# Kernel tuning notes

Measured on AMD Instinct MI355X. Metric: run time of the kernel, lower is better.

Reference implementation:

```python
import jax, jax.numpy as jnp
import numpy as np

V, E, H = 50257, 512, 1024
B, S = 64, 512


def setup_inputs() -> dict:
    key = jax.random.key(0)
    ks = jax.random.split(key, 12)
    return {
        "inp": jax.random.randint(ks[0], (B,), 0, V),
        "hidden": jax.random.normal(ks[1], (1, B, H), dtype=jnp.float32),
        "encoder_outputs": jax.random.normal(ks[2], (B, S, H), dtype=jnp.float32),
        "emb": jax.random.normal(ks[3], (V, E), dtype=jnp.float32) * 0.02,
        "W": jax.random.uniform(ks[4], (H, H), dtype=jnp.float32) - 0.5,
        "U": jax.random.uniform(ks[5], (H, H), dtype=jnp.float32) - 0.5,
        "v": jax.random.uniform(ks[6], (H, 1), dtype=jnp.float32) - 0.5,
        "W_ih": jax.random.normal(ks[7], (H, E), dtype=jnp.float32) * 0.02,
        "W_hh": jax.random.normal(ks[8], (H, H), dtype=jnp.float32) * 0.02,
        "b_ih": jnp.zeros((H,), dtype=jnp.float32),
        "b_hh": jnp.zeros((H,), dtype=jnp.float32),
        "out_W": jax.random.normal(ks[9], (V, H), dtype=jnp.float32) * 0.02,
        "out_b": jnp.zeros((V,), dtype=jnp.float32),
    }


def reference(inp, hidden, encoder_outputs, emb, W, U, v, W_ih, W_hh, b_ih, b_hh, out_W, out_b):
    # Embedding lookup: (B, E)
    x = emb[inp]
    # Bahdanau additive attention. last decoder state: hidden[0] -> (B, H)
    Wh = jnp.einsum('ij,bsj->bis', W, encoder_outputs)        # (B, H, S)
    Uh = jnp.einsum('ij,bj->bi', U, hidden[0])[:, :, None]    # (B, H, 1)
    e = jnp.einsum('h,bhs->bs', v[:, 0], jnp.tanh(Wh + Uh))   # (B, S)
    alpha = jax.nn.softmax(e, axis=-1)                        # exp_e / sum(exp_e)
    context = jnp.einsum('bs,bsh->bh', alpha, encoder_outputs)  # (B, H)
    # Single-step tanh RNN with the attention context as initial hidden state
    h = jnp.tanh(x @ W_ih.T + b_ih + context @ W_hh.T + b_hh)  # (B, H)
    logits = h @ out_W.T + out_b                                # (B, V)
    # Match torch shapes: rnn_output (B,1,H) -> logits (B,1,V); h_n (1,B,H)
    return logits[:, None, :], h[None, :, :]
```

## Files before the change

### kernel.cpp

```cpp
#include <hip/hip_runtime.h>
#include <hip/hip_bf16.h>
#include <stdint.h>

#define DEVINL __device__ __forceinline__

typedef __bf16 bf16x8 __attribute__((ext_vector_type(8)));
typedef float  f32x4  __attribute__((ext_vector_type(4)));
typedef unsigned int uint2v __attribute__((ext_vector_type(2)));
typedef unsigned int uint4v __attribute__((ext_vector_type(4)));
typedef unsigned short ushort_t;

#define VSZ   50257
#define EDIM  512
#define HDIM  1024
#define BATCH 64
#define SEQ   512


DEVINL f32x4 MF(bf16x8 a, bf16x8 b, f32x4 c) {
  return __builtin_amdgcn_mfma_f32_16x16x32_bf16(a, b, c, 0, 0, 0);
}

DEVINL bf16x8 ldfrag(const short* buf, int row, int k) {
  uint4v t = *(const uint4v*)&buf[row * 64 + (k ^ ((row & 7) << 3))];
  return __builtin_bit_cast(bf16x8, t);
}

DEVINL void split4(f32x4 w, uint2v& hv, uint2v& lv) {
  unsigned u0 = __float_as_uint(w.x), u1 = __float_as_uint(w.y);
  unsigned u2 = __float_as_uint(w.z), u3 = __float_as_uint(w.w);
  unsigned h0 = u0 & 0xFFFF0000u, h1 = u1 & 0xFFFF0000u;
  unsigned h2 = u2 & 0xFFFF0000u, h3 = u3 & 0xFFFF0000u;
  hv.x = (h0 >> 16) | h1;
  hv.y = (h2 >> 16) | h3;
  float l0 = w.x - __uint_as_float(h0);
  float l1 = w.y - __uint_as_float(h1);
  float l2 = w.z - __uint_as_float(h2);
  float l3 = w.w - __uint_as_float(h3);
  lv.x = (__float_as_uint(l0) >> 16) | (__float_as_uint(l1) & 0xFFFF0000u);
  lv.y = (__float_as_uint(l2) >> 16) | (__float_as_uint(l3) & 0xFFFF0000u);
}

DEVINL uint2v packhi4_rn(f32x4 w) {
  unsigned u0 = __float_as_uint(w.x), u1 = __float_as_uint(w.y);
  unsigned u2 = __float_as_uint(w.z), u3 = __float_as_uint(w.w);
  unsigned r0 = u0 + 0x7FFFu + ((u0 >> 16) & 1u);
  unsigned r1 = u1 + 0x7FFFu + ((u1 >> 16) & 1u);
  unsigned r2 = u2 + 0x7FFFu + ((u2 >> 16) & 1u);
  unsigned r3 = u3 + 0x7FFFu + ((u3 >> 16) & 1u);
  uint2v o;
  o.x = (r0 >> 16) | (r1 & 0xFFFF0000u);
  o.y = (r2 >> 16) | (r3 & 0xFFFF0000u);
  return o;
}

DEVINL float fast_tanh(float s) {
  float e2 = __expf(2.0f * s);
  return 1.0f - 2.0f * __builtin_amdgcn_rcpf(e2 + 1.0f);
}

__global__ __launch_bounds__(256) void prep_w_kernel(const float* __restrict__ W,
                                                     ushort_t* __restrict__ Whi,
                                                     ushort_t* __restrict__ Wlo) {
  int idx4 = blockIdx.x * 256 + threadIdx.x;
  f32x4 w = *(const f32x4*)&W[(size_t)idx4 * 4];
  uint2v hv, lv;
  split4(w, hv, lv);
  ((uint2v*)Whi)[idx4] = hv;
  ((uint2v*)Wlo)[idx4] = lv;
}

__global__ __launch_bounds__(256) void uh_kernel(const float* __restrict__ U,
                                                 const float* __restrict__ hidden,
                                                 float* __restrict__ Uh) {
  int wid = threadIdx.x >> 6, lane = threadIdx.x & 63;
  int i = blockIdx.x * 4 + wid;
  const float* Urow = U + (size_t)i * HDIM;
  float acc[64];
#pragma unroll
  for (int b = 0; b < 64; ++b) acc[b] = 0.0f;
  for (int t = 0; t < HDIM / 64; ++t) {
    float w = Urow[t * 64 + lane];
#pragma unroll
    for (int b = 0; b < 64; ++b)
      acc[b] += w * hidden[(size_t)b * HDIM + t * 64 + lane];
  }
#pragma unroll
  for (int mask = 1; mask <= 32; mask <<= 1)
#pragma unroll
    for (int b = 0; b < 64; ++b) acc[b] += __shfl_xor(acc[b], mask, 64);
  if (lane == 0) {
#pragma unroll
    for (int b = 0; b < 64; ++b) Uh[(size_t)b * HDIM + i] = acc[b];
  }
}

__global__ __launch_bounds__(256) void e_kernel(const float* __restrict__ enc,
                                                const ushort_t* __restrict__ Whi,
                                                const ushort_t* __restrict__ Wlo,
                                                const float* __restrict__ Uh,
                                                const float* __restrict__ v,
                                                float* __restrict__ e_parts) {
  __shared__ short Ahi[128 * 64], Alo[128 * 64], Bhi[128 * 64], Blo[128 * 64];
  __shared__ float ewave[2][2][64];

  const int t = threadIdx.x;
  const int i0 = blockIdx.x * 128;
  const int bs0 = blockIdx.y * 128;
  const int wid = t >> 6, lane = t & 63, r = lane & 15, g = lane >> 4;
  const int wr = wid >> 1, wc = wid & 1;

  f32x4 z4 = {0.f, 0.f, 0.f, 0.f};
  f32x4 acc[4][4];
#pragma unroll
  for (int m = 0; m < 4; ++m)
#pragma unroll
    for (int n = 0; n < 4; ++n) acc[m][n] = z4;

  for (int kt = 0; kt < 16; ++kt) {
    __syncthreads();
#pragma unroll
    for (int rep = 0; rep < 8; ++rep) {
      int p = rep * 256 + t;
      int row = p >> 4, c = p & 15;
      f32x4 w = *(const f32x4*)&enc[(size_t)(bs0 + row) * HDIM + kt * 64 + c * 4];
      uint2v hv, lv;
      split4(w, hv, lv);
      int idx = row * 64 + ((c * 4) ^ ((row & 7) << 3));
      *(uint2v*)&Ahi[idx] = hv;
      *(uint2v*)&Alo[idx] = lv;
    }
#pragma unroll
    for (int rep = 0; rep < 4; ++rep) {
      int p = rep * 256 + t;
      int row = p >> 3, c = p & 7;
      int idx = row * 64 + ((c * 8) ^ ((row & 7) << 3));
      *(uint4v*)&Bhi[idx] = *(const uint4v*)&Whi[(size_t)(i0 + row) * HDIM + kt * 64 + c * 8];
      *(uint4v*)&Blo[idx] = *(const uint4v*)&Wlo[(size_t)(i0 + row) * HDIM + kt * 64 + c * 8];
    }
    __syncthreads();
#pragma unroll
    for (int ks = 0; ks < 2; ++ks) {
      int k = ks * 32 + g * 8;
      bf16x8 ah[4], al[4], bh[4], bl[4];
#pragma unroll
      for (int m = 0; m < 4; ++m) {
        int arow = wr * 64 + m * 16 + r;
        ah[m] = ldfrag(Ahi, arow, k);
        al[m] = ldfrag(Alo, arow, k);
        int brow = wc * 64 + m * 16 + r;
        bh[m] = ldfrag(Bhi, brow, k);
        bl[m] = ldfrag(Blo, brow, k);
      }
#pragma unroll
      for (int m = 0; m < 4; ++m)
#pragma unroll
        for (int n = 0; n < 4; ++n) {
          acc[m][n] = MF(ah[m], bh[n], acc[m][n]);
          acc[m][n] = MF(ah[m], bl[n], acc[m][n]);
          acc[m][n] = MF(al[m], bh[n], acc[m][n]);
        }
    }
  }

  const int b = bs0 >> 9;
  float uhv[4], vv[4];
#pragma unroll
  for (int n = 0; n < 4; ++n) {
    int col = i0 + wc * 64 + n * 16 + r;
    uhv[n] = Uh[(size_t)b * HDIM + col];
    vv[n] = v[col];
  }
  float esum[16];
#pragma unroll
  for (int q = 0; q < 16; ++q) esum[q] = 0.0f;
#pragma unroll
  for (int m = 0; m < 4; ++m)
#pragma unroll
    for (int n = 0; n < 4; ++n)
#pragma unroll
      for (int j = 0; j < 4; ++j) {
        float s = acc[m][n][j] + uhv[n];
        esum[m * 4 + j] += fast_tanh(s) * vv[n];
      }
#pragma unroll
  for (int mask = 1; mask <= 8; mask <<= 1)
#pragma unroll
    for (int q = 0; q < 16; ++q) esum[q] += __shfl_xor(esum[q], mask, 64);
  if (r == 0) {
#pragma unroll
    for (int m = 0; m < 4; ++m)
#pragma unroll
      for (int j = 0; j < 4; ++j)
        ewave[wr][wc][m * 16 + g * 4 + j] = esum[m * 4 + j];
  }
  __syncthreads();
  if (t < 128) {
    int w2 = t >> 6, rr = t & 63;
    e_parts[(size_t)blockIdx.x * 32768 + bs0 + w2 * 64 + rr] =
        ewave[w2][0][rr] + ewave[w2][1][rr];
  }
}

__global__ __launch_bounds__(256) void softmax_kernel(const float* __restrict__ e_parts,
                                                      float* __restrict__ alpha) {
  __shared__ float red[256];
  int b = blockIdx.x, t = threadIdx.x;
  float ev0 = 0.f, ev1 = 0.f;
#pragma unroll
  for (int nc = 0; nc < 8; ++nc) {
    ev0 += e_parts[(size_t)nc * 32768 + b * SEQ + t];
    ev1 += e_parts[(size_t)nc * 32768 + b * SEQ + t + 256];
  }
  red[t] = fmaxf(ev0, ev1);
  __syncthreads();
  for (int off = 128; off > 0; off >>= 1) {
    if (t < off) red[t] = fmaxf(red[t], red[t + off]);
    __syncthreads();
  }
  float mx = red[0];
  __syncthreads();
  float x0 = __expf(ev0 - mx), x1 = __expf(ev1 - mx);
  red[t] = x0 + x1;
  __syncthreads();
  for (int off = 128; off > 0; off >>= 1) {
    if (t < off) red[t] += red[t + off];
    __syncthreads();
  }
  float inv = 1.0f / red[0];
  alpha[b * SEQ + t] = x0 * inv;
  alpha[b * SEQ + t + 256] = x1 * inv;
}

__global__ __launch_bounds__(256) void ctx_kernel(const float* __restrict__ alpha,
                                                  const float* __restrict__ enc,
                                                  float* __restrict__ ctx_parts) {
  int b = blockIdx.x, q = blockIdx.y, t = threadIdx.x;
  f32x4 acc = {0.f, 0.f, 0.f, 0.f};
  for (int s = q * 128; s < q * 128 + 128; ++s) {
    float a = alpha[b * SEQ + s];
    f32x4 ev = *(const f32x4*)&enc[((size_t)b * SEQ + s) * HDIM + t * 4];
    acc.x += a * ev.x; acc.y += a * ev.y; acc.z += a * ev.z; acc.w += a * ev.w;
  }
  *(f32x4*)&ctx_parts[((size_t)q * BATCH + b) * HDIM + t * 4] = acc;
}

__global__ __launch_bounds__(256) void ctx_reduce_kernel(const float* __restrict__ ctx_parts,
                                                         float* __restrict__ ctx) {
  int idx = blockIdx.x * 256 + threadIdx.x;
  const f32x4* p = (const f32x4*)ctx_parts;
  f32x4 s0 = p[idx];
  f32x4 s1 = p[idx + 16384];
  f32x4 s2 = p[idx + 32768];
  f32x4 s3 = p[idx + 49152];
  f32x4 r;
  r.x = s0.x + s1.x + s2.x + s3.x;
  r.y = s0.y + s1.y + s2.y + s3.y;
  r.z = s0.z + s1.z + s2.z + s3.z;
  r.w = s0.w + s1.w + s2.w + s3.w;
  ((f32x4*)ctx)[idx] = r;
}

__global__ __launch_bounds__(256) void rnn_kernel(const int* __restrict__ inp,
                                                  const float* __restrict__ emb,
                                                  const float* __restrict__ Wih,
                                                  const float* __restrict__ Whh,
                                                  const float* __restrict__ bih,
                                                  const float* __restrict__ bhh,
                                                  const float* __restrict__ ctx,
                                                  float* __restrict__ h_out,
                                                  ushort_t* __restrict__ h_bf16) {
  int wid = threadIdx.x >> 6, lane = threadIdx.x & 63;
  int i = blockIdx.x * 4 + wid;
  float acc[64];
#pragma unroll
  for (int b = 0; b < 64; ++b) acc[b] = 0.0f;
  const float* w1 = Wih + (size_t)i * EDIM;
  for (int t = 0; t < EDIM / 64; ++t) {
    float w = w1[t * 64 + lane];
#pragma unroll
    for (int b = 0; b < 64; ++b)
      acc[b] += w * emb[(size_t)inp[b] * EDIM + t * 64 + lane];
  }
  const float* w2 = Whh + (size_t)i * HDIM;
  for (int t = 0; t < HDIM / 64; ++t) {
    float w = w2[t * 64 + lane];
#pragma unroll
    for (int b = 0; b < 64; ++b)
      acc[b] += w * ctx[(size_t)b * HDIM + t * 64 + lane];
  }
#pragma unroll
  for (int mask = 1; mask <= 32; mask <<= 1)
#pragma unroll
    for (int b = 0; b < 64; ++b) acc[b] += __shfl_xor(acc[b], mask, 64);
  if (lane == 0) {
    float bias = bih[i] + bhh[i];
#pragma unroll
    for (int b = 0; b < 64; ++b) {
      float hv = fast_tanh(acc[b] + bias);
      h_out[(size_t)b * HDIM + i] = hv;
      unsigned u = __float_as_uint(hv);
      h_bf16[(size_t)b * HDIM + i] = (ushort_t)((u + 0x7FFFu + ((u >> 16) & 1u)) >> 16);
    }
  }
}

__global__ __launch_bounds__(256) void logits_kernel(const ushort_t* __restrict__ hbf,
                                                     const float* __restrict__ outW,
                                                     const float* __restrict__ outb,
                                                     float* __restrict__ out) {
  __shared__ short As[64 * 64];
  __shared__ short Bs[128 * 64];
  const int t = threadIdx.x;
  const int n0 = blockIdx.x * 128;
  const int wid = t >> 6, lane = t & 63, r = lane & 15, g = lane >> 4;

  f32x4 z4 = {0.f, 0.f, 0.f, 0.f};
  f32x4 acc[4][2];
#pragma unroll
  for (int m = 0; m < 4; ++m) {
    acc[m][0] = z4;
    acc[m][1] = z4;
  }

  for (int kt = 0; kt < 16; ++kt) {
    __syncthreads();
#pragma unroll
    for (int rep = 0; rep < 2; ++rep) {
      int p = rep * 256 + t;
      int row = p >> 3, c = p & 7;
      *(uint4v*)&As[row * 64 + ((c * 8) ^ ((row & 7) << 3))] =
          *(const uint4v*)&hbf[(size_t)row * HDIM + kt * 64 + c * 8];
    }
#pragma unroll
    for (int rep = 0; rep < 8; ++rep) {
      int p = rep * 256 + t;
      int row = p >> 4, c = p & 15;
      int gr = n0 + row;
      f32x4 wv = z4;
      if (gr < VSZ) wv = *(const f32x4*)&outW[(size_t)gr * HDIM + kt * 64 + c * 4];
      *(uint2v*)&Bs[row * 64 + ((c * 4) ^ ((row & 7) << 3))] = packhi4_rn(wv);
    }
    __syncthreads();
#pragma unroll
    for (int ks = 0; ks < 2; ++ks) {
      int k = ks * 32 + g * 8;
      bf16x8 a[4], bb[2];
#pragma unroll
      for (int m = 0; m < 4; ++m) a[m] = ldfrag(As, m * 16 + r, k);
#pragma unroll
      for (int n = 0; n < 2; ++n) bb[n] = ldfrag(Bs, wid * 32 + n * 16 + r, k);
#pragma unroll
      for (int m = 0; m < 4; ++m)
#pragma unroll
        for (int n = 0; n < 2; ++n) acc[m][n] = MF(a[m], bb[n], acc[m][n]);
    }
  }
#pragma unroll
  for (int n = 0; n < 2; ++n) {
    int col = n0 + wid * 32 + n * 16 + r;
    if (col < VSZ) {
      float ob = outb[col];
#pragma unroll
      for (int m = 0; m < 4; ++m)
#pragma unroll
        for (int j = 0; j < 4; ++j) {
          int row = m * 16 + g * 4 + j;
          out[(size_t)row * VSZ + col] = acc[m][n][j] + ob;
        }
    }
  }
}

extern "C" void kernel_launch(void* const* d_in, const int* in_sizes, int n_in,
                              void* d_out, int out_size, void* d_ws, size_t ws_size,
                              hipStream_t stream) {
  const int* inp = (const int*)d_in[0];
  const float* hidden = (const float*)d_in[1];
  const float* enc = (const float*)d_in[2];
  const float* emb = (const float*)d_in[3];
  const float* W = (const float*)d_in[4];
  const float* U = (const float*)d_in[5];
  const float* v = (const float*)d_in[6];
  const float* Wih = (const float*)d_in[7];
  const float* Whh = (const float*)d_in[8];
  const float* bih = (const float*)d_in[9];
  const float* bhh = (const float*)d_in[10];
  const float* outW = (const float*)d_in[11];
  const float* outb = (const float*)d_in[12];
  float* out = (float*)d_out;

  char* ws = (char*)d_ws;
  ushort_t* Whi = (ushort_t*)(ws + 0);
  ushort_t* Wlo = (ushort_t*)(ws + 2097152);
  float* Uh = (float*)(ws + 4194304);
  float* e_parts = (float*)(ws + 4456448);
  float* alpha = (float*)(ws + 5505024);
  float* ctx_parts = (float*)(ws + 5636096);
  float* ctx = (float*)(ws + 6684672);
  ushort_t* hbf = (ushort_t*)(ws + 6946816);

  prep_w_kernel<<<1024, 256, 0, stream>>>(W, Whi, Wlo);
  uh_kernel<<<256, 256, 0, stream>>>(U, hidden, Uh);
  e_kernel<<<dim3(8, 256), 256, 0, stream>>>(enc, Whi, Wlo, Uh, v, e_parts);
  softmax_kernel<<<64, 256, 0, stream>>>(e_parts, alpha);
  ctx_kernel<<<dim3(64, 4), 256, 0, stream>>>(alpha, enc, ctx_parts);
  ctx_reduce_kernel<<<64, 256, 0, stream>>>(ctx_parts, ctx);
  rnn_kernel<<<256, 256, 0, stream>>>(inp, emb, Wih, Whh, bih, bhh, ctx,
                                      out + (size_t)BATCH * VSZ, hbf);
  logits_kernel<<<(VSZ + 127) / 128, 256, 0, stream>>>(hbf, outW, outb, out);
}
```

Measured before the change: 1.022 ms.

## Shrink e_kernel K-tile with padded LDS, widen ctx grid, halve logits tile

Three separate changes. The attention-score GEMM moves from 64-wide K tiles with XOR swizzle to 32-wide K tiles in padded rows of stride 40, which cuts LDS use so more blocks can be resident, at the cost of twice as many sync rounds. The context reduction gets 4x more blocks by also splitting along the hidden dimension, with scalar loads and four independent accumulators. The logits GEMM halves its N tile to 64 columns, doubling the block count for more parallelism but reloading the hidden-state tile more often.

Measured after the change: 832.7 us. 1.23x faster.

```diff
diff --git a/kernel.cpp b/kernel.cpp
--- a/kernel.cpp
+++ b/kernel.cpp
@@ -19,6 +19,11 @@
 
 DEVINL f32x4 MF(bf16x8 a, bf16x8 b, f32x4 c) {
   return __builtin_amdgcn_mfma_f32_16x16x32_bf16(a, b, c, 0, 0, 0);
+}
+
+DEVINL bf16x8 ldfrag40(const short* buf, int row, int k) {
+  uint4v t = *(const uint4v*)&buf[row * 40 + k];
+  return __builtin_bit_cast(bf16x8, t);
 }
 
 DEVINL bf16x8 ldfrag(const short* buf, int row, int k) {
@@ -101,7 +106,7 @@
                                                 const float* __restrict__ Uh,
                                                 const float* __restrict__ v,
                                                 float* __restrict__ e_parts) {
-  __shared__ short Ahi[128 * 64], Alo[128 * 64], Bhi[128 * 64], Blo[128 * 64];
+  __shared__ short Ahi[128 * 40], Alo[128 * 40], Bhi[128 * 40], Blo[128 * 40];
   __shared__ float ewave[2][2][64];
 
   const int t = threadIdx.x;
@@ -117,40 +122,39 @@
 #pragma unroll
     for (int n = 0; n < 4; ++n) acc[m][n] = z4;
 
-  for (int kt = 0; kt < 16; ++kt) {
-    __syncthreads();
-#pragma unroll
-    for (int rep = 0; rep < 8; ++rep) {
-      int p = rep * 256 + t;
-      int row = p >> 4, c = p & 15;
-      f32x4 w = *(const f32x4*)&enc[(size_t)(bs0 + row) * HDIM + kt * 64 + c * 4];
-      uint2v hv, lv;
-      split4(w, hv, lv);
-      int idx = row * 64 + ((c * 4) ^ ((row & 7) << 3));
-      *(uint2v*)&Ahi[idx] = hv;
-      *(uint2v*)&Alo[idx] = lv;
-    }
+  for (int kt = 0; kt < 32; ++kt) {
+    __syncthreads();
 #pragma unroll
     for (int rep = 0; rep < 4; ++rep) {
       int p = rep * 256 + t;
       int row = p >> 3, c = p & 7;
-      int idx = row * 64 + ((c * 8) ^ ((row & 7) << 3));
-      *(uint4v*)&Bhi[idx] = *(const uint4v*)&Whi[(size_t)(i0 + row) * HDIM + kt * 64 + c * 8];
-      *(uint4v*)&Blo[idx] = *(const uint4v*)&Wlo[(size_t)(i0 + row) * HDIM + kt * 64 + c * 8];
-    }
-    __syncthreads();
-#pragma unroll
-    for (int ks = 0; ks < 2; ++ks) {
-      int k = ks * 32 + g * 8;
+      f32x4 w = *(const f32x4*)&enc[(size_t)(bs0 + row) * HDIM + kt * 32 + c * 4];
+      uint2v hv, lv;
+      split4(w, hv, lv);
+      int idx = row * 40 + c * 4;
+      *(uint2v*)&Ahi[idx] = hv;
+      *(uint2v*)&Alo[idx] = lv;
+    }
+#pragma unroll
+    for (int rep = 0; rep < 2; ++rep) {
+      int p = rep * 256 + t;
+      int row = p >> 2, c = p & 3;
+      int idx = row * 40 + c * 8;
+      *(uint4v*)&Bhi[idx] = *(const uint4v*)&Whi[(size_t)(i0 + row) * HDIM + kt * 32 + c * 8];
+      *(uint4v*)&Blo[idx] = *(const uint4v*)&Wlo[(size_t)(i0 + row) * HDIM + kt * 32 + c * 8];
+    }
+    __syncthreads();
+    {
+      int k = g * 8;
       bf16x8 ah[4], al[4], bh[4], bl[4];
 #pragma unroll
       for (int m = 0; m < 4; ++m) {
         int arow = wr * 64 + m * 16 + r;
-        ah[m] = ldfrag(Ahi, arow, k);
-        al[m] = ldfrag(Alo, arow, k);
+        ah[m] = ldfrag40(Ahi, arow, k);
+        al[m] = ldfrag40(Alo, arow, k);
         int brow = wc * 64 + m * 16 + r;
-        bh[m] = ldfrag(Bhi, brow, k);
-        bl[m] = ldfrag(Blo, brow, k);
+        bh[m] = ldfrag40(Bhi, brow, k);
+        bl[m] = ldfrag40(Blo, brow, k);
       }
 #pragma unroll
       for (int m = 0; m < 4; ++m)
@@ -235,14 +239,21 @@
 __global__ __launch_bounds__(256) void ctx_kernel(const float* __restrict__ alpha,
                                                   const float* __restrict__ enc,
                                                   float* __restrict__ ctx_parts) {
-  int b = blockIdx.x, q = blockIdx.y, t = threadIdx.x;
-  f32x4 acc = {0.f, 0.f, 0.f, 0.f};
-  for (int s = q * 128; s < q * 128 + 128; ++s) {
-    float a = alpha[b * SEQ + s];
-    f32x4 ev = *(const f32x4*)&enc[((size_t)b * SEQ + s) * HDIM + t * 4];
-    acc.x += a * ev.x; acc.y += a * ev.y; acc.z += a * ev.z; acc.w += a * ev.w;
-  }
-  *(f32x4*)&ctx_parts[((size_t)q * BATCH + b) * HDIM + t * 4] = acc;
+  int b = blockIdx.x, qs = blockIdx.y, qh = blockIdx.z, t = threadIdx.x;
+  int h = qh * 256 + t;
+  float a0 = 0.f, a1 = 0.f, a2 = 0.f, a3 = 0.f;
+  int s0 = qs * 128;
+  for (int s = s0; s < s0 + 128; s += 4) {
+    float w0 = alpha[b * SEQ + s + 0];
+    float w1 = alpha[b * SEQ + s + 1];
+    float w2 = alpha[b * SEQ + s + 2];
+    float w3 = alpha[b * SEQ + s + 3];
+    a0 += w0 * enc[((size_t)b * SEQ + s + 0) * HDIM + h];
+    a1 += w1 * enc[((size_t)b * SEQ + s + 1) * HDIM + h];
+    a2 += w2 * enc[((size_t)b * SEQ + s + 2) * HDIM + h];
+    a3 += w3 * enc[((size_t)b * SEQ + s + 3) * HDIM + h];
+  }
+  ctx_parts[((size_t)qs * BATCH + b) * HDIM + h] = (a0 + a1) + (a2 + a3);
 }
 
 __global__ __launch_bounds__(256) void ctx_reduce_kernel(const float* __restrict__ ctx_parts,
@@ -310,18 +321,15 @@
                                                      const float* __restrict__ outb,
                                                      float* __restrict__ out) {
   __shared__ short As[64 * 64];
-  __shared__ short Bs[128 * 64];
+  __shared__ short Bs[64 * 64];
   const int t = threadIdx.x;
-  const int n0 = blockIdx.x * 128;
+  const int n0 = blockIdx.x * 64;
   const int wid = t >> 6, lane = t & 63, r = lane & 15, g = lane >> 4;
 
   f32x4 z4 = {0.f, 0.f, 0.f, 0.f};
-  f32x4 acc[4][2];
-#pragma unroll
-  for (int m = 0; m < 4; ++m) {
-    acc[m][0] = z4;
-    acc[m][1] = z4;
-  }
+  f32x4 acc[4];
+#pragma unroll
+  for (int m = 0; m < 4; ++m) acc[m] = z4;
 
   for (int kt = 0; kt < 16; ++kt) {
     __syncthreads();
@@ -333,7 +341,7 @@
           *(const uint4v*)&hbf[(size_t)row * HDIM + kt * 64 + c * 8];
     }
 #pragma unroll
-    for (int rep = 0; rep < 8; ++rep) {
+    for (int rep = 0; rep < 4; ++rep) {
       int p = rep * 256 + t;
       int row = p >> 4, c = p & 15;
       int gr = n0 + row;
@@ -345,20 +353,16 @@
 #pragma unroll
     for (int ks = 0; ks < 2; ++ks) {
       int k = ks * 32 + g * 8;
-      bf16x8 a[4], bb[2];
+      bf16x8 a[4], bb;
 #pragma unroll
       for (int m = 0; m < 4; ++m) a[m] = ldfrag(As, m * 16 + r, k);
-#pragma unroll
-      for (int n = 0; n < 2; ++n) bb[n] = ldfrag(Bs, wid * 32 + n * 16 + r, k);
-#pragma unroll
-      for (int m = 0; m < 4; ++m)
-#pragma unroll
-        for (int n = 0; n < 2; ++n) acc[m][n] = MF(a[m], bb[n], acc[m][n]);
-    }
-  }
-#pragma unroll
-  for (int n = 0; n < 2; ++n) {
-    int col = n0 + wid * 32 + n * 16 + r;
+      bb = ldfrag(Bs, wid * 16 + r, k);
+#pragma unroll
+      for (int m = 0; m < 4; ++m) acc[m] = MF(a[m], bb, acc[m]);
+    }
+  }
+  {
+    int col = n0 + wid * 16 + r;
     if (col < VSZ) {
       float ob = outb[col];
 #pragma unroll
@@ -366,7 +370,7 @@
 #pragma unroll
         for (int j = 0; j < 4; ++j) {
           int row = m * 16 + g * 4 + j;
-          out[(size_t)row * VSZ + col] = acc[m][n][j] + ob;
+          out[(size_t)row * VSZ + col] = acc[m][j] + ob;
         }
     }
   }
@@ -404,9 +408,9 @@
   uh_kernel<<<256, 256, 0, stream>>>(U, hidden, Uh);
   e_kernel<<<dim3(8, 256), 256, 0, stream>>>(enc, Whi, Wlo, Uh, v, e_parts);
   softmax_kernel<<<64, 256, 0, stream>>>(e_parts, alpha);
-  ctx_kernel<<<dim3(64, 4), 256, 0, stream>>>(alpha, enc, ctx_parts);
+  ctx_kernel<<<dim3(64, 4, 4), 256, 0, stream>>>(alpha, enc, ctx_parts);
   ctx_reduce_kernel<<<64, 256, 0, stream>>>(ctx_parts, ctx);
   rnn_kernel<<<256, 256, 0, stream>>>(inp, emb, Wih, Whh, bih, bhh, ctx,
                                       out + (size_t)BATCH * VSZ, hbf);
-  logits_kernel<<<(VSZ + 127) / 128, 256, 0, stream>>>(hbf, outW, outb, out);
-}
+  logits_kernel<<<(VSZ + 63) / 64, 256, 0, stream>>>(hbf, outW, outb, out);
+}
```
